# Kernel optimization log

Hardware: AMD Instinct MI355X
Metric: run time of the kernel (lower is better)

The kernel has to match this reference:

```python
import jax, jax.numpy as jnp
import numpy as np

D_MODEL = 1024

def setup_inputs() -> dict:
    key = jax.random.key(0)
    ks = jax.random.split(key, 7)
    s = 1.0 / np.sqrt(D_MODEL)
    x = jax.random.normal(ks[0], (4, 2048, D_MODEL), dtype=jnp.float32)
    Wq = jax.random.normal(ks[1], (D_MODEL, D_MODEL), dtype=jnp.float32) * s
    Wk = jax.random.normal(ks[2], (D_MODEL, D_MODEL), dtype=jnp.float32) * s
    Wv = jax.random.normal(ks[3], (D_MODEL, D_MODEL), dtype=jnp.float32) * s
    bq = jax.random.normal(ks[4], (D_MODEL,), dtype=jnp.float32) * 0.01
    bk = jax.random.normal(ks[5], (D_MODEL,), dtype=jnp.float32) * 0.01
    bv = jax.random.normal(ks[6], (D_MODEL,), dtype=jnp.float32) * 0.01
    return {"x": x, "Wq": Wq, "bq": bq, "Wk": Wk, "bk": bk, "Wv": Wv, "bv": bv}

def reference(x, Wq, bq, Wk, bk, Wv, bv):
    # Linear layers: y = x @ W^T + b (torch nn.Linear convention)
    q = jnp.einsum('bsd,ed->bse', x, Wq) + bq
    k = jnp.einsum('bsd,ed->bse', x, Wk) + bk
    v = jnp.einsum('bsd,ed->bse', x, Wv) + bv
    scale = 1.0 / jnp.sqrt(jnp.asarray(k.shape[-1], dtype=x.dtype))
    scores = jnp.einsum('bqd,bkd->bqk', q, k) * scale  # [B, S, S]
    attn = jax.nn.softmax(scores, axis=-1)
    return jnp.einsum('bqk,bkd->bqd', attn, v)
```

## Files before the change

kernel.cpp:

```cpp
#include <hip/hip_runtime.h>
#include <cstdint>


typedef unsigned short u16;
typedef __attribute__((ext_vector_type(4))) float f32x4;
typedef __attribute__((ext_vector_type(8))) __bf16 bf16x8;

#define AS1(p) ((const __attribute__((address_space(1))) void*)(p))
#define AS3(p) ((__attribute__((address_space(3))) void*)(p))

#define SEQ 2048
#define DM 1024

template <int N> struct ic { static constexpr int v = N; };

__device__ __forceinline__ u16 f2b(float f) {
  uint32_t u = __builtin_bit_cast(uint32_t, f);
  u += 0x7FFFu + ((u >> 16) & 1u);
  return (u16)(u >> 16);
}
__device__ __forceinline__ float b2f(uint32_t bits16) {
  return __builtin_bit_cast(float, bits16 << 16);
}

__global__ __launch_bounds__(256) void cvt_x_kernel(const float* __restrict__ x,
                                                    u16* __restrict__ xb) {
  int i = (blockIdx.x * 256 + threadIdx.x) * 4;
  float4 v = *(const float4*)(x + i);
  ushort4 o;
  o.x = f2b(v.x); o.y = f2b(v.y); o.z = f2b(v.z); o.w = f2b(v.w);
  *(ushort4*)(xb + i) = o;
}

__global__ __launch_bounds__(256) void pack_w_kernel(const float* __restrict__ Wq,
                                                     const float* __restrict__ Wk,
                                                     const float* __restrict__ Wv,
                                                     u16* __restrict__ wcat) {
  int i = (blockIdx.x * 256 + threadIdx.x) * 4;
  const float* src;
  int j;
  if (i < (1 << 20))      { src = Wq; j = i; }
  else if (i < (2 << 20)) { src = Wk; j = i - (1 << 20); }
  else                    { src = Wv; j = i - (2 << 20); }
  float4 v = *(const float4*)(src + j);
  ushort4 o;
  o.x = f2b(v.x); o.y = f2b(v.y); o.z = f2b(v.z); o.w = f2b(v.w);
  *(ushort4*)(wcat + i) = o;
}


template <int FM, int FN, int WGM, int WGN, int T, int RING>
__device__ __forceinline__ void gemm_engine(const u16* __restrict__ A,
                                            const u16* __restrict__ Bt,
                                            int lda, int ldb, char* lds,
                                            f32x4 (&acc)[FM][FN], int tid) {
  constexpr int NPH = 2 * T;
  constexpr int RA  = WGM * FM * 16, RB = WGN * FN * 16;
  constexpr int SZA = RA * 64, SZB = RB * 64;
  constexpr int JA  = RA / 128, JB = RB / 128;
  constexpr int LPH = JA + JB;
  constexpr int WS  = (RING - 3) * LPH;
  static_assert(NPH > RING, "need at least one steady phase");

  char* ldsA = lds;
  char* ldsB = lds + RING * SZA;

  const int l = tid & 63, w = tid >> 6;
  const int wm = w / WGN, wn = w % WGN;
  const int fr = l & 15, ch = l >> 4;
  const int tb = ((fr >> 1) << 7) + (((((fr & 1) << 2) | ch) ^ (fr >> 1)) << 4);
  const int wmoff = wm * (FM * 1024), wnoff = wn * (FN * 1024);
  const int wbase = (tid & ~63) * 16;

  int aoff[JA], boff[JB];
#pragma unroll
  for (int j = 0; j < JA; ++j) {
    int o  = j * 8192 + tid * 16;
    int rp = o >> 7;
    int cl = ((o >> 4) & 7) ^ (rp & 7);
    aoff[j] = (rp * 2 + (cl >> 2)) * lda + (cl & 3) * 8;
  }
#pragma unroll
  for (int j = 0; j < JB; ++j) {
    int o  = j * 8192 + tid * 16;
    int rp = o >> 7;
    int cl = ((o >> 4) & 7) ^ (rp & 7);
    boff[j] = (rp * 2 + (cl >> 2)) * ldb + (cl & 3) * 8;
  }

  auto stage = [&](int regS, int ke) {
#pragma unroll
    for (int j = 0; j < JA; ++j)
      __builtin_amdgcn_global_load_lds(AS1(A + aoff[j] + ke),
          AS3(ldsA + regS * SZA + j * 8192 + wbase), 16, 0, 0);
#pragma unroll
    for (int j = 0; j < JB; ++j)
      __builtin_amdgcn_global_load_lds(AS1(Bt + boff[j] + ke),
          AS3(ldsB + regS * SZB + j * 8192 + wbase), 16, 0, 0);
  };

  auto phase = [&](auto Wc, auto Sc, int regR, int regS, int keS) {
    constexpr int  WV = decltype(Wc)::v;
    constexpr bool SV = (decltype(Sc)::v != 0);
    if constexpr (SV) stage(regS, keS);
    const char* la = ldsA + regR * SZA + wmoff + tb;
    const char* lb = ldsB + regR * SZB + wnoff + tb;
    bf16x8 af[FM], bfr[FN];
#pragma unroll
    for (int m = 0; m < FM; ++m) af[m] = *(const bf16x8*)(la + m * 1024);
#pragma unroll
    for (int n = 0; n < FN; ++n) bfr[n] = *(const bf16x8*)(lb + n * 1024);
    asm volatile("s_waitcnt vmcnt(%0)" :: "i"(WV) : "memory");
    __builtin_amdgcn_s_barrier();
    asm volatile("s_waitcnt lgkmcnt(0)" ::: "memory");
    __builtin_amdgcn_sched_barrier(0);
    __builtin_amdgcn_s_setprio(1);
#pragma unroll
    for (int m = 0; m < FM; ++m)
#pragma unroll
      for (int n = 0; n < FN; ++n)
        acc[m][n] = __builtin_amdgcn_mfma_f32_16x16x32_bf16(af[m], bfr[n],
                                                            acc[m][n], 0, 0, 0);
    __builtin_amdgcn_s_setprio(0);
  };

#pragma unroll
  for (int p = 0; p < RING - 2; ++p) stage(p, p * 32);
#pragma unroll
  for (int m = 0; m < FM; ++m)
#pragma unroll
    for (int n = 0; n < FN; ++n)
#pragma unroll
      for (int j = 0; j < 4; ++j) acc[m][n][j] = 0.f;
  asm volatile("s_waitcnt vmcnt(%0)" :: "i"(WS) : "memory");
  __builtin_amdgcn_s_barrier();

  int regR = 0, regS = RING - 2, keS = (RING - 2) * 32;
  auto adv = [&](int& r) { r = (r + 1 == RING) ? 0 : r + 1; };

  for (int hp = 0; hp < NPH - RING; ++hp) {
    phase(ic<WS>{}, ic<1>{}, regR, regS, keS);
    adv(regR); adv(regS); keS += 32;
  }
  if constexpr (RING == 4) {
    phase(ic<WS>{}, ic<1>{}, regR, regS, keS); adv(regR); adv(regS); keS += 32;
    phase(ic<WS>{}, ic<1>{}, regR, regS, keS); adv(regR);
    phase(ic<0>{},  ic<0>{}, regR, 0, 0);      adv(regR);
    phase(ic<0>{},  ic<0>{}, regR, 0, 0);
  } else {
    phase(ic<WS>{},      ic<1>{}, regR, regS, keS); adv(regR); adv(regS); keS += 32;
    phase(ic<WS>{},      ic<1>{}, regR, regS, keS); adv(regR);
    phase(ic<2 * LPH>{}, ic<0>{}, regR, 0, 0);      adv(regR);
    phase(ic<LPH>{},     ic<0>{}, regR, 0, 0);      adv(regR);
    phase(ic<0>{},       ic<0>{}, regR, 0, 0);      adv(regR);
    phase(ic<0>{},       ic<0>{}, regR, 0, 0);
  }
}

__global__ __launch_bounds__(512, 2) void qkv_gemm(const u16* __restrict__ xb,
                                                   const u16* __restrict__ wcat,
                                                   const float* __restrict__ bq,
                                                   const float* __restrict__ bk,
                                                   const float* __restrict__ bv,
                                                   u16* __restrict__ qb,
                                                   u16* __restrict__ kb,
                                                   u16* __restrict__ vtb) {
  __shared__ __align__(16) char lds[131072];
  const int tid = threadIdx.x;
  const int lin = blockIdx.x;
  const int wgid = (lin & 7) * 48 + (lin >> 3);
  const int bx = wgid % 12, by = wgid / 12;
  const int bm = by * 256, bn = bx * 256;
  f32x4 acc[8][4];
  gemm_engine<8, 4, 2, 4, 16, 4>(xb + bm * 1024, wcat + bn * 1024, 1024, 1024,
                                 lds, acc, tid);
  const int l = tid & 63, w = tid >> 6;
  const int wm = w >> 2, wn = w & 3;
  const int which = bn >> 10;
  const float* bias = (which == 0) ? bq : (which == 1) ? bk : bv;
#pragma unroll
  for (int m = 0; m < 8; ++m)
#pragma unroll
    for (int n = 0; n < 4; ++n) {
      int col = bn + wn * 64 + n * 16 + (l & 15);
      int e = col & 1023;
      float bval = bias[e];
#pragma unroll
      for (int j = 0; j < 4; ++j) {
        int row = bm + wm * 128 + m * 16 + (l >> 4) * 4 + j;
        u16 hb = f2b(acc[m][n][j] + bval);
        if (which == 0)      qb[row * 1024 + e] = hb;
        else if (which == 1) kb[row * 1024 + e] = hb;
        else { int b = row >> 11, s = row & 2047; vtb[(b << 21) + e * 2048 + s] = hb; }
      }
    }
}

__global__ __launch_bounds__(512, 2) void scores_gemm(const u16* __restrict__ qb,
                                                      const u16* __restrict__ kb,
                                                      u16* __restrict__ sb) {
  __shared__ __align__(16) char lds[131072];
  const int tid = threadIdx.x;
  const int lin = blockIdx.x;
  const int wgid = (lin & 7) * 32 + (lin >> 3);
  const int b = wgid >> 6, r = wgid & 63;
  const int by = r >> 3, bx = r & 7;
  const int bm = by * 256, bn = bx * 256;
  f32x4 acc[8][4];
  gemm_engine<8, 4, 2, 4, 16, 4>(qb + b * (SEQ * DM) + bm * 1024,
                                 kb + b * (SEQ * DM) + bn * 1024, 1024, 1024,
                                 lds, acc, tid);
  u16* out = sb + (size_t)b * SEQ * SEQ;
  const int l = tid & 63, w = tid >> 6;
  const int wm = w >> 2, wn = w & 3;
#pragma unroll
  for (int m = 0; m < 8; ++m)
#pragma unroll
    for (int n = 0; n < 4; ++n) {
      int col = bn + wn * 64 + n * 16 + (l & 15);
#pragma unroll
      for (int j = 0; j < 4; ++j) {
        int row = bm + wm * 128 + m * 16 + (l >> 4) * 4 + j;
        out[row * 2048 + col] = f2b(acc[m][n][j] * 0.03125f);
      }
    }
}

__global__ __launch_bounds__(256) void softmax_k(const u16* __restrict__ sb,
                                                 u16* __restrict__ pb) {
  __shared__ float red[8];
  int row = blockIdx.x;
  const u16* src = sb + (size_t)row * 2048;
  u16* dst = pb + (size_t)row * 2048;
  int t = threadIdx.x;
  uint4 raw = *(const uint4*)(src + t * 8);
  uint32_t rw[4] = {raw.x, raw.y, raw.z, raw.w};
  float v[8];
#pragma unroll
  for (int q = 0; q < 4; ++q) {
    v[2 * q]     = b2f(rw[q] & 0xFFFFu);
    v[2 * q + 1] = __builtin_bit_cast(float, rw[q] & 0xFFFF0000u);
  }
  float m = v[0];
#pragma unroll
  for (int j = 1; j < 8; ++j) m = fmaxf(m, v[j]);
  for (int off = 32; off; off >>= 1) m = fmaxf(m, __shfl_xor(m, off));
  int w = t >> 6, l = t & 63;
  if (l == 0) red[w] = m;
  __syncthreads();
  m = fmaxf(fmaxf(red[0], red[1]), fmaxf(red[2], red[3]));
  float e[8], s = 0.f;
#pragma unroll
  for (int j = 0; j < 8; ++j) { e[j] = __expf(v[j] - m); s += e[j]; }
  for (int off = 32; off; off >>= 1) s += __shfl_xor(s, off);
  if (l == 0) red[4 + w] = s;
  __syncthreads();
  s = (red[4] + red[5]) + (red[6] + red[7]);
  float inv = 1.0f / s;
  uint32_t o[4];
#pragma unroll
  for (int q = 0; q < 4; ++q) {
    uint32_t lo = f2b(e[2 * q] * inv);
    uint32_t hi = f2b(e[2 * q + 1] * inv);
    o[q] = lo | (hi << 16);
  }
  *(uint4*)(dst + t * 8) = make_uint4(o[0], o[1], o[2], o[3]);
}

__global__ __launch_bounds__(512, 2) void pv_gemm(const u16* __restrict__ pb,
                                                  const u16* __restrict__ vtb,
                                                  float* __restrict__ out) {
  __shared__ __align__(16) char lds[147456];
  const int tid = threadIdx.x;
  const int lin = blockIdx.x;
  const int wgid = (lin & 7) * 32 + (lin >> 3);
  const int b = wgid >> 6, r = wgid & 63;
  const int by = r >> 2, bx = r & 3;
  const int bm = by * 128, bn = bx * 256;
  f32x4 acc[4][4];
  gemm_engine<4, 4, 2, 4, 32, 6>(pb + (size_t)b * SEQ * SEQ + bm * 2048,
                                 vtb + (size_t)b * DM * SEQ + bn * 2048,
                                 2048, 2048, lds, acc, tid);
  float* o = out + (size_t)b * SEQ * DM;
  const int l = tid & 63, w = tid >> 6;
  const int wm = w >> 2, wn = w & 3;
#pragma unroll
  for (int m = 0; m < 4; ++m)
#pragma unroll
    for (int n = 0; n < 4; ++n) {
      int col = bn + wn * 64 + n * 16 + (l & 15);
#pragma unroll
      for (int j = 0; j < 4; ++j) {
        int row = bm + wm * 64 + m * 16 + (l >> 4) * 4 + j;
        o[row * 1024 + col] = acc[m][n][j];
      }
    }
}

extern "C" void kernel_launch(void* const* d_in, const int* in_sizes, int n_in,
                              void* d_out, int out_size, void* d_ws, size_t ws_size,
                              hipStream_t stream) {
  const float* x  = (const float*)d_in[0];
  const float* Wq = (const float*)d_in[1];
  const float* bq = (const float*)d_in[2];
  const float* Wk = (const float*)d_in[3];
  const float* bk = (const float*)d_in[4];
  const float* Wv = (const float*)d_in[5];
  const float* bv = (const float*)d_in[6];
  float* out = (float*)d_out;

  char* ws = (char*)d_ws;
  u16* xb   = (u16*)(ws);
  u16* wcat = (u16*)(ws + 16777216);
  u16* qb   = (u16*)(ws + 23068672);
  u16* kb   = (u16*)(ws + 39845888);
  u16* vtb  = (u16*)(ws + 56623104);
  u16* sb   = (u16*)(ws + 73400320);
  u16* pb   = (u16*)(ws + 106954752);

  cvt_x_kernel<<<8192, 256, 0, stream>>>(x, xb);
  pack_w_kernel<<<3072, 256, 0, stream>>>(Wq, Wk, Wv, wcat);
  qkv_gemm<<<384, 512, 0, stream>>>(xb, wcat, bq, bk, bv, qb, kb, vtb);
  scores_gemm<<<256, 512, 0, stream>>>(qb, kb, sb);
  softmax_k<<<8192, 256, 0, stream>>>(sb, pb);
  pv_gemm<<<256, 512, 0, stream>>>(pb, vtb, out);
}
```

Measured before the change: 187.3 us.

## Replace ring-buffered GEMM engine with double-buffered 64-K tile, four-quadrant ping-pong schedule

Replaces the 4/6-deep ring of 32-wide K phases with a double-buffered 64-wide K tile. Each tile is split into four MFMA quadrants, with barriers between them and the global-to-LDS loads for later tiles interleaved across the quadrants. The LDS layout changes to a new XOR swizzle, and pv_gemm's LDS allocation shrinks. The aim is better overlap of loads with MFMA and fewer waits per K step, at the cost of more barriers per tile and a more fragile vmcnt accounting.

Measured after the change: 188.6 us. No clear change (+0.7%).

```diff
diff --git a/kernel.cpp b/kernel.cpp
--- a/kernel.cpp
+++ b/kernel.cpp
@@ -49,112 +49,136 @@
 }
 
 
-template <int FM, int FN, int WGM, int WGN, int T, int RING>
-__device__ __forceinline__ void gemm_engine(const u16* __restrict__ A,
-                                            const u16* __restrict__ Bt,
-                                            int lda, int ldb, char* lds,
-                                            f32x4 (&acc)[FM][FN], int tid) {
-  constexpr int NPH = 2 * T;
-  constexpr int RA  = WGM * FM * 16, RB = WGN * FN * 16;
-  constexpr int SZA = RA * 64, SZB = RB * 64;
-  constexpr int JA  = RA / 128, JB = RB / 128;
-  constexpr int LPH = JA + JB;
-  constexpr int WS  = (RING - 3) * LPH;
-  static_assert(NPH > RING, "need at least one steady phase");
+#define BAR()  __builtin_amdgcn_s_barrier()
+#define LGK0() do { asm volatile("s_waitcnt lgkmcnt(0)" ::: "memory"); \
+                    __builtin_amdgcn_sched_barrier(0); } while (0)
+
+template <int FM, int T>
+__device__ __forceinline__ void gemm8p(const u16* __restrict__ A,
+                                       const u16* __restrict__ Bt,
+                                       int lda, int ldb, char* lds,
+                                       f32x4 (&acc)[FM][4], int tid) {
+  constexpr int MH  = FM / 2;
+  constexpr int SZA = FM * 4096;
+  constexpr int VMS = (FM == 8) ? 6 : 4;
 
   char* ldsA = lds;
-  char* ldsB = lds + RING * SZA;
-
-  const int l = tid & 63, w = tid >> 6;
-  const int wm = w / WGN, wn = w % WGN;
+  char* ldsB = lds + 2 * SZA;
+
+  const int l  = tid & 63, w = tid >> 6;
+  const int wm = w >> 2, wn = w & 3;
   const int fr = l & 15, ch = l >> 4;
-  const int tb = ((fr >> 1) << 7) + (((((fr & 1) << 2) | ch) ^ (fr >> 1)) << 4);
-  const int wmoff = wm * (FM * 1024), wnoff = wn * (FN * 1024);
-  const int wbase = (tid & ~63) * 16;
-
-  int aoff[JA], boff[JB];
-#pragma unroll
-  for (int j = 0; j < JA; ++j) {
-    int o  = j * 8192 + tid * 16;
-    int rp = o >> 7;
-    int cl = ((o >> 4) & 7) ^ (rp & 7);
-    aoff[j] = (rp * 2 + (cl >> 2)) * lda + (cl & 3) * 8;
+  const int laneq  = fr * 128 + ((ch ^ (fr & 7)) << 4);
+  const int aslot0 = (FM == 8) ? wm * 16384 : wm * 8192;
+  const int bslot0 = (wn >> 1) * 16384 + (wn & 1) * 8192;
+
+  const int srow  = tid >> 3;
+  const int sclog = (tid & 7) ^ ((tid >> 3) & 7);
+  const u16* gA = A + srow * lda + sclog * 8;
+  const u16* gB = Bt + srow * ldb + sclog * 8;
+  const int wlin = w * 1024;
+
+  auto stageA = [&](int mh, int t) {
+#pragma unroll
+    for (int j = 0; j < 2; ++j)
+      __builtin_amdgcn_global_load_lds(
+          AS1(gA + (mh * 128 + j * 64) * lda + t * 64),
+          AS3(ldsA + (t & 1) * SZA + ((FM == 8) ? mh * 16384 : 0) + j * 8192 + wlin),
+          16, 0, 0);
+  };
+  auto stageB = [&](int bh, int t) {
+#pragma unroll
+    for (int j = 0; j < 2; ++j)
+      __builtin_amdgcn_global_load_lds(
+          AS1(gB + (bh * 128 + j * 64) * ldb + t * 64),
+          AS3(ldsB + (t & 1) * 32768 + bh * 16384 + j * 8192 + wlin),
+          16, 0, 0);
+  };
+
+  auto readA = [&](bf16x8 (&dst)[FM], int msub, int db) {
+#pragma unroll
+    for (int mf = 0; mf < MH; ++mf)
+#pragma unroll
+      for (int kk = 0; kk < 2; ++kk)
+        dst[mf * 2 + kk] = *(const bf16x8*)(ldsA + db * SZA + aslot0 +
+                                            msub * MH * 2048 + mf * 2048 +
+                                            (laneq ^ (kk << 6)));
+  };
+  auto readB = [&](bf16x8 (&dst)[4], int nsub, int db) {
+#pragma unroll
+    for (int nf = 0; nf < 2; ++nf)
+#pragma unroll
+      for (int kk = 0; kk < 2; ++kk)
+        dst[nf * 2 + kk] = *(const bf16x8*)(ldsB + db * 32768 + bslot0 +
+                                            nsub * 4096 + nf * 2048 +
+                                            (laneq ^ (kk << 6)));
+  };
+
+  auto mfmaQ = [&](int msub, int nsub, bf16x8 (&a)[FM], bf16x8 (&b)[4]) {
+    __builtin_amdgcn_s_setprio(1);
+#pragma unroll
+    for (int mf = 0; mf < MH; ++mf)
+#pragma unroll
+      for (int nf = 0; nf < 2; ++nf)
+#pragma unroll
+        for (int kk = 0; kk < 2; ++kk)
+          acc[msub * MH + mf][nsub * 2 + nf] =
+              __builtin_amdgcn_mfma_f32_16x16x32_bf16(
+                  a[mf * 2 + kk], b[nf * 2 + kk],
+                  acc[msub * MH + mf][nsub * 2 + nf], 0, 0, 0);
+    __builtin_amdgcn_s_setprio(0);
+  };
+
+  auto tile = [&](auto p1s, auto p234s, auto vmw, int t) {
+    constexpr bool P1S  = (decltype(p1s)::v != 0);
+    constexpr bool P23S = (decltype(p234s)::v != 0);
+    constexpr int  VMW  = decltype(vmw)::v;
+    const int db = t & 1;
+    bf16x8 alo[FM], ahi[FM], blo[4], bhi[4];
+    readA(alo, 0, db); readB(blo, 0, db);
+    if constexpr (P1S) stageB(1, t + 1);
+    BAR(); LGK0();
+    mfmaQ(0, 0, alo, blo);
+    BAR();
+    readB(bhi, 1, db);
+    BAR(); LGK0();
+    mfmaQ(0, 1, alo, bhi);
+    BAR();
+    readA(ahi, 1, db);
+    if constexpr (P23S) stageB(0, t + 2);
+    BAR(); LGK0();
+    mfmaQ(1, 1, ahi, bhi);
+    BAR();
+    if constexpr (P23S) {
+      stageA(0, t + 2);
+      if constexpr (FM == 8) stageA(1, t + 2);
+    }
+    if constexpr (VMW >= 0)
+      asm volatile("s_waitcnt vmcnt(%0)" :: "i"(VMW) : "memory");
+    BAR(); LGK0();
+    mfmaQ(1, 0, ahi, blo);
+    BAR();
+  };
+
+#pragma unroll
+  for (int tt = 0; tt < 2; ++tt) {
+    if constexpr (FM == 8) { stageA(0, tt); stageB(0, tt); stageA(1, tt); stageB(1, tt); }
+    else                   { stageA(0, tt); stageB(0, tt); stageB(1, tt); }
   }
 #pragma unroll
-  for (int j = 0; j < JB; ++j) {
-    int o  = j * 8192 + tid * 16;
-    int rp = o >> 7;
-    int cl = ((o >> 4) & 7) ^ (rp & 7);
-    boff[j] = (rp * 2 + (cl >> 2)) * ldb + (cl & 3) * 8;
-  }
-
-  auto stage = [&](int regS, int ke) {
-#pragma unroll
-    for (int j = 0; j < JA; ++j)
-      __builtin_amdgcn_global_load_lds(AS1(A + aoff[j] + ke),
-          AS3(ldsA + regS * SZA + j * 8192 + wbase), 16, 0, 0);
-#pragma unroll
-    for (int j = 0; j < JB; ++j)
-      __builtin_amdgcn_global_load_lds(AS1(Bt + boff[j] + ke),
-          AS3(ldsB + regS * SZB + j * 8192 + wbase), 16, 0, 0);
-  };
-
-  auto phase = [&](auto Wc, auto Sc, int regR, int regS, int keS) {
-    constexpr int  WV = decltype(Wc)::v;
-    constexpr bool SV = (decltype(Sc)::v != 0);
-    if constexpr (SV) stage(regS, keS);
-    const char* la = ldsA + regR * SZA + wmoff + tb;
-    const char* lb = ldsB + regR * SZB + wnoff + tb;
-    bf16x8 af[FM], bfr[FN];
-#pragma unroll
-    for (int m = 0; m < FM; ++m) af[m] = *(const bf16x8*)(la + m * 1024);
-#pragma unroll
-    for (int n = 0; n < FN; ++n) bfr[n] = *(const bf16x8*)(lb + n * 1024);
-    asm volatile("s_waitcnt vmcnt(%0)" :: "i"(WV) : "memory");
-    __builtin_amdgcn_s_barrier();
-    asm volatile("s_waitcnt lgkmcnt(0)" ::: "memory");
-    __builtin_amdgcn_sched_barrier(0);
-    __builtin_amdgcn_s_setprio(1);
-#pragma unroll
-    for (int m = 0; m < FM; ++m)
-#pragma unroll
-      for (int n = 0; n < FN; ++n)
-        acc[m][n] = __builtin_amdgcn_mfma_f32_16x16x32_bf16(af[m], bfr[n],
-                                                            acc[m][n], 0, 0, 0);
-    __builtin_amdgcn_s_setprio(0);
-  };
-
-#pragma unroll
-  for (int p = 0; p < RING - 2; ++p) stage(p, p * 32);
-#pragma unroll
   for (int m = 0; m < FM; ++m)
 #pragma unroll
-    for (int n = 0; n < FN; ++n)
+    for (int n = 0; n < 4; ++n)
 #pragma unroll
       for (int j = 0; j < 4; ++j) acc[m][n][j] = 0.f;
-  asm volatile("s_waitcnt vmcnt(%0)" :: "i"(WS) : "memory");
-  __builtin_amdgcn_s_barrier();
-
-  int regR = 0, regS = RING - 2, keS = (RING - 2) * 32;
-  auto adv = [&](int& r) { r = (r + 1 == RING) ? 0 : r + 1; };
-
-  for (int hp = 0; hp < NPH - RING; ++hp) {
-    phase(ic<WS>{}, ic<1>{}, regR, regS, keS);
-    adv(regR); adv(regS); keS += 32;
-  }
-  if constexpr (RING == 4) {
-    phase(ic<WS>{}, ic<1>{}, regR, regS, keS); adv(regR); adv(regS); keS += 32;
-    phase(ic<WS>{}, ic<1>{}, regR, regS, keS); adv(regR);
-    phase(ic<0>{},  ic<0>{}, regR, 0, 0);      adv(regR);
-    phase(ic<0>{},  ic<0>{}, regR, 0, 0);
-  } else {
-    phase(ic<WS>{},      ic<1>{}, regR, regS, keS); adv(regR); adv(regS); keS += 32;
-    phase(ic<WS>{},      ic<1>{}, regR, regS, keS); adv(regR);
-    phase(ic<2 * LPH>{}, ic<0>{}, regR, 0, 0);      adv(regR);
-    phase(ic<LPH>{},     ic<0>{}, regR, 0, 0);      adv(regR);
-    phase(ic<0>{},       ic<0>{}, regR, 0, 0);      adv(regR);
-    phase(ic<0>{},       ic<0>{}, regR, 0, 0);
-  }
+  asm volatile("s_waitcnt vmcnt(%0)" :: "i"((FM == 8) ? 8 : 6) : "memory");
+  BAR();
+
+  tile(ic<0>{}, ic<1>{}, ic<VMS>{}, 0);
+  for (int t = 1; t <= T - 3; ++t)
+    tile(ic<1>{}, ic<1>{}, ic<VMS>{}, t);
+  tile(ic<1>{}, ic<0>{}, ic<0>{}, T - 2);
+  tile(ic<0>{}, ic<0>{}, ic<-1>{}, T - 1);
 }
 
 __global__ __launch_bounds__(512, 2) void qkv_gemm(const u16* __restrict__ xb,
@@ -172,8 +196,7 @@
   const int bx = wgid % 12, by = wgid / 12;
   const int bm = by * 256, bn = bx * 256;
   f32x4 acc[8][4];
-  gemm_engine<8, 4, 2, 4, 16, 4>(xb + bm * 1024, wcat + bn * 1024, 1024, 1024,
-                                 lds, acc, tid);
+  gemm8p<8, 16>(xb + bm * 1024, wcat + bn * 1024, 1024, 1024, lds, acc, tid);
   const int l = tid & 63, w = tid >> 6;
   const int wm = w >> 2, wn = w & 3;
   const int which = bn >> 10;
@@ -207,9 +230,8 @@
   const int by = r >> 3, bx = r & 7;
   const int bm = by * 256, bn = bx * 256;
   f32x4 acc[8][4];
-  gemm_engine<8, 4, 2, 4, 16, 4>(qb + b * (SEQ * DM) + bm * 1024,
-                                 kb + b * (SEQ * DM) + bn * 1024, 1024, 1024,
-                                 lds, acc, tid);
+  gemm8p<8, 16>(qb + b * (SEQ * DM) + bm * 1024,
+                kb + b * (SEQ * DM) + bn * 1024, 1024, 1024, lds, acc, tid);
   u16* out = sb + (size_t)b * SEQ * SEQ;
   const int l = tid & 63, w = tid >> 6;
   const int wm = w >> 2, wn = w & 3;
@@ -270,7 +292,7 @@
 __global__ __launch_bounds__(512, 2) void pv_gemm(const u16* __restrict__ pb,
                                                   const u16* __restrict__ vtb,
                                                   float* __restrict__ out) {
-  __shared__ __align__(16) char lds[147456];
+  __shared__ __align__(16) char lds[98304];
   const int tid = threadIdx.x;
   const int lin = blockIdx.x;
   const int wgid = (lin & 7) * 32 + (lin >> 3);
@@ -278,9 +300,9 @@
   const int by = r >> 2, bx = r & 3;
   const int bm = by * 128, bn = bx * 256;
   f32x4 acc[4][4];
-  gemm_engine<4, 4, 2, 4, 32, 6>(pb + (size_t)b * SEQ * SEQ + bm * 2048,
-                                 vtb + (size_t)b * DM * SEQ + bn * 2048,
-                                 2048, 2048, lds, acc, tid);
+  gemm8p<4, 32>(pb + (size_t)b * SEQ * SEQ + bm * 2048,
+                vtb + (size_t)b * DM * SEQ + bn * 2048, 2048, 2048,
+                lds, acc, tid);
   float* o = out + (size_t)b * SEQ * DM;
   const int l = tid & 63, w = tid >> 6;
   const int wm = w >> 2, wn = w & 3;
```
